# Kernel tuning notes

Measured on AMD Instinct MI355X. Metric: run time of the kernel, lower is better.

The kernel has to match this reference:

```python
import jax, jax.numpy as jnp
import numpy as np

N_PREV = 8191
DIMS = 4096


def setup_inputs() -> dict:
    key = jax.random.key(0)
    k1, k2, k3, k4, k5 = jax.random.split(key, 5)
    prev_inps = jax.random.normal(k1, (N_PREV, DIMS), dtype=jnp.float32)
    inp = jax.random.normal(k2, (DIMS,), dtype=jnp.float32)
    # learned parameters, init std=0.01 as in the torch module
    W_Q = jax.random.normal(k3, (DIMS, DIMS), dtype=jnp.float32) * 0.01
    W_K = jax.random.normal(k4, (DIMS, DIMS), dtype=jnp.float32) * 0.01
    W_V = jax.random.normal(k5, (DIMS, DIMS), dtype=jnp.float32) * 0.01
    return {"prev_inps": prev_inps, "inp": inp, "W_Q": W_Q, "W_K": W_K, "W_V": W_V}


def reference(prev_inps, inp, W_Q, W_K, W_V):
    # One masked self-attention decode step.
    inputs = jnp.concatenate([prev_inps, inp[None, :]], axis=0)  # (n+1, d)
    query = W_Q @ inp                                            # (d,)
    keys = jnp.einsum('md,nd->nm', W_K, inputs)                  # (n+1, d)
    values = jnp.einsum('md,nd->nm', W_V, inputs)                # (n+1, d)
    logits = keys @ query                                        # (n+1,)
    aweights = jax.nn.softmax(logits, axis=-1)                   # (n+1,)
    context = aweights @ values                                  # (d,)
    output = context + inp                                       # residual
    return (output, inputs)
```

## Files before the change

### kernel.cpp

```cpp
#include <hip/hip_runtime.h>
#include <math.h>

#define D      4096
#define NPREV  8191
#define NROWS  8192
#define FB     512
#define FR     (NROWS / FB)

typedef float f4 __attribute__((ext_vector_type(4)));

static __device__ __forceinline__ f4 nt_load4(const float* p) {
    return __builtin_nontemporal_load(reinterpret_cast<const f4*>(p));
}
static __device__ __forceinline__ void nt_store4(f4 v, float* p) {
    __builtin_nontemporal_store(v, reinterpret_cast<f4*>(p));
}
static __device__ __forceinline__ f4 ld4(const float* p) {
    return *reinterpret_cast<const f4*>(p);
}
static __device__ __forceinline__ void st4(f4 v, float* p) {
    *reinterpret_cast<f4*>(p) = v;
}

template<bool RESIDUAL>
__global__ void k_matvec_rows(const float* __restrict__ W, const float* __restrict__ v,
                              const float* __restrict__ resid, float* __restrict__ out) {
    int row  = blockIdx.x * 4 + (threadIdx.x >> 6);
    int lane = threadIdx.x & 63;
    const float* Wrow = W + (size_t)row * D;
    float acc = 0.f;
    #pragma unroll
    for (int i = 0; i < 16; ++i) {
        int c = lane + i * 64;
        f4 w = nt_load4(Wrow + 4 * c);
        f4 x = ld4(v + 4 * c);
        acc += w.x * x.x + w.y * x.y + w.z * x.z + w.w * x.w;
    }
    #pragma unroll
    for (int off = 32; off; off >>= 1) acc += __shfl_down(acc, off, 64);
    if (lane == 0) out[row] = RESIDUAL ? (acc + resid[row]) : acc;
}

__global__ void k_kq(const float* __restrict__ W, const float* __restrict__ q,
                     float* __restrict__ kq) {
    __shared__ float s_q[D];
    __shared__ f4 s_part[64][4];
    int t = threadIdx.x;
    int b = blockIdx.x;
    for (int i = t; i < D; i += 256) s_q[i] = q[i];
    __syncthreads();
    int c4 = b * 4 + (t & 3);
    int r0 = t >> 2;
    f4 acc = (f4)0.f;
    #pragma unroll 16
    for (int i = 0; i < 64; ++i) {
        int m = r0 + i * 64;
        acc += s_q[m] * nt_load4(W + (size_t)m * D + 4 * c4);
    }
    s_part[r0][t & 3] = acc;
    __syncthreads();
    if (t < 4) {
        f4 a = (f4)0.f;
        #pragma unroll
        for (int g = 0; g < 64; ++g) a += s_part[g][t];
        st4(a, kq + 4 * (b * 4 + t));
    }
}

__global__ __launch_bounds__(1024, 4) void k_flash(
        const float* __restrict__ prev, const float* __restrict__ inp,
        const float* __restrict__ kq, float* __restrict__ io,
        float* __restrict__ ms, float* __restrict__ ctxpart) {
    __shared__ float s_wred[16][FR];
    __shared__ float s_log[FR];
    const int n0 = blockIdx.x * FR;
    const int t = threadIdx.x;
    const int wid = t >> 6, lane = t & 63;
    const f4 kqv = ld4(kq + 4 * t);

    f4 x[FR];
    #pragma unroll
    for (int r = 0; r < FR; ++r) {
        int n = n0 + r;
        const float* src = (n < NPREV) ? (prev + (size_t)n * D) : inp;
        x[r] = ld4(src + 4 * t);
    }
    float p[FR];
    #pragma unroll
    for (int r = 0; r < FR; ++r) {
        int n = n0 + r;
        nt_store4(x[r], io + (size_t)n * D + 4 * t);
        p[r] = x[r].x * kqv.x + x[r].y * kqv.y + x[r].z * kqv.z + x[r].w * kqv.w;
    }
    #pragma unroll
    for (int r = 0; r < FR; ++r) {
        float v = p[r];
        #pragma unroll
        for (int off = 32; off; off >>= 1) v += __shfl_down(v, off, 64);
        if (lane == 0) s_wred[wid][r] = v;
    }
    __syncthreads();
    if (t < FR) {
        float s = 0.f;
        #pragma unroll
        for (int w = 0; w < 16; ++w) s += s_wred[w][t];
        s_log[t] = s;
    }
    __syncthreads();
    float m_b = -INFINITY;
    #pragma unroll
    for (int r = 0; r < FR; ++r) m_b = fmaxf(m_b, s_log[r]);
    float e[FR], s_b = 0.f;
    #pragma unroll
    for (int r = 0; r < FR; ++r) { e[r] = __expf(s_log[r] - m_b); s_b += e[r]; }
    f4 a = (f4)0.f;
    #pragma unroll
    for (int r = 0; r < FR; ++r) a += e[r] * x[r];
    st4(a, ctxpart + (size_t)blockIdx.x * D + 4 * t);
    if (t == 0) { ms[2 * blockIdx.x] = m_b; ms[2 * blockIdx.x + 1] = s_b; }
}

__global__ void k_combine(const float* __restrict__ ms, const float* __restrict__ ctxpart,
                          float* __restrict__ ctx) {
    __shared__ float s_w[FB];
    __shared__ float s_red[12];
    __shared__ f4 s_acc[8][32];
    int t = threadIdx.x;
    int lane = t & 63, wid = t >> 6;
    float m0 = ms[2 * t], m1 = ms[2 * (t + 256)];
    float mx = fmaxf(m0, m1);
    #pragma unroll
    for (int off = 32; off; off >>= 1) mx = fmaxf(mx, __shfl_down(mx, off, 64));
    if (lane == 0) s_red[wid] = mx;
    __syncthreads();
    float M = fmaxf(fmaxf(s_red[0], s_red[1]), fmaxf(s_red[2], s_red[3]));
    float w0 = __expf(m0 - M), w1 = __expf(m1 - M);
    s_w[t] = w0; s_w[t + 256] = w1;
    float sc = w0 * ms[2 * t + 1] + w1 * ms[2 * (t + 256) + 1];
    #pragma unroll
    for (int off = 32; off; off >>= 1) sc += __shfl_down(sc, off, 64);
    if (lane == 0) s_red[8 + wid] = sc;
    __syncthreads();
    float S = s_red[8] + s_red[9] + s_red[10] + s_red[11];
    int c  = t & 31;
    int g8 = t >> 5;
    int col4 = blockIdx.x * 32 + c;
    f4 a = (f4)0.f;
    #pragma unroll 8
    for (int i = 0; i < 64; ++i) {
        int p = g8 * 64 + i;
        a += s_w[p] * ld4(ctxpart + (size_t)p * D + 4 * col4);
    }
    s_acc[g8][c] = a;
    __syncthreads();
    if (t < 32) {
        f4 aa = (f4)0.f;
        #pragma unroll
        for (int g = 0; g < 8; ++g) aa += s_acc[g][t];
        st4(aa * (1.f / S), ctx + 4 * (blockIdx.x * 32 + t));
    }
}

extern "C" void kernel_launch(void* const* d_in, const int* in_sizes, int n_in,
                              void* d_out, int out_size, void* d_ws, size_t ws_size,
                              hipStream_t stream) {
    const float* prev = (const float*)d_in[0];
    const float* inp  = (const float*)d_in[1];
    const float* W_Q  = (const float*)d_in[2];
    const float* W_K  = (const float*)d_in[3];
    const float* W_V  = (const float*)d_in[4];
    float* out = (float*)d_out;
    float* io  = out + D;
    float* ws  = (float*)d_ws;

    float* q       = ws;
    float* kq      = q + D;
    float* ms      = kq + D;
    float* ctxpart = ms + 2 * FB;
    float* ctx     = ctxpart + (size_t)FB * D;

    k_matvec_rows<false><<<1024, 256, 0, stream>>>(W_Q, inp, nullptr, q);
    k_kq<<<256, 256, 0, stream>>>(W_K, q, kq);
    k_flash<<<FB, 1024, 0, stream>>>(prev, inp, kq, io, ms, ctxpart);
    k_combine<<<32, 256, 0, stream>>>(ms, ctxpart, ctx);
    k_matvec_rows<true><<<1024, 256, 0, stream>>>(W_V, ctx, inp, out);
}
```

Baseline: 116.0 us.

## Split flash pass into more, smaller LDS-staged blocks with workspace-size fallback

The flash-decode pass now uses 2048 blocks of 4 rows each instead of 512 blocks of 16. Rows are staged in shared memory rather than held in registers, and launch bounds allow 8 blocks per CU, aiming for more parallelism and memory-level concurrency on the large prev_inps read and write. The trade-off is 2048 partial context vectors (32 MB) to write and then read back in the combine kernel, which is generalised to a template and uses 64 blocks. If the workspace is too small, the old 16-row register path runs instead.

Result: faster. 112.5 us (-3.0%).

```diff
diff --git a/kernel.cpp b/kernel.cpp
--- a/kernel.cpp
+++ b/kernel.cpp
@@ -4,8 +4,6 @@
 #define D      4096
 #define NPREV  8191
 #define NROWS  8192
-#define FB     512
-#define FR     (NROWS / FB)
 
 typedef float f4 __attribute__((ext_vector_type(4)));
 
@@ -67,40 +65,98 @@
     }
 }
 
-__global__ __launch_bounds__(1024, 4) void k_flash(
+#define FBL  2048
+#define FRL  4
+__global__ __launch_bounds__(1024, 8) void k_flash_lds(
         const float* __restrict__ prev, const float* __restrict__ inp,
         const float* __restrict__ kq, float* __restrict__ io,
         float* __restrict__ ms, float* __restrict__ ctxpart) {
-    __shared__ float s_wred[16][FR];
-    __shared__ float s_log[FR];
-    const int n0 = blockIdx.x * FR;
+    __shared__ f4 s_x[FRL][1024];
+    __shared__ float s_wred[16][FRL];
+    __shared__ float s_log[FRL];
+    const int n0 = blockIdx.x * FRL;
     const int t = threadIdx.x;
     const int wid = t >> 6, lane = t & 63;
     const f4 kqv = ld4(kq + 4 * t);
 
-    f4 x[FR];
-    #pragma unroll
-    for (int r = 0; r < FR; ++r) {
+    f4 x[FRL];
+    #pragma unroll
+    for (int r = 0; r < FRL; ++r) {
         int n = n0 + r;
         const float* src = (n < NPREV) ? (prev + (size_t)n * D) : inp;
         x[r] = ld4(src + 4 * t);
     }
-    float p[FR];
-    #pragma unroll
-    for (int r = 0; r < FR; ++r) {
+    float p[FRL];
+    #pragma unroll
+    for (int r = 0; r < FRL; ++r) {
+        int n = n0 + r;
+        nt_store4(x[r], io + (size_t)n * D + 4 * t);
+        s_x[r][t] = x[r];
+        p[r] = x[r].x * kqv.x + x[r].y * kqv.y + x[r].z * kqv.z + x[r].w * kqv.w;
+    }
+    #pragma unroll
+    for (int r = 0; r < FRL; ++r) {
+        float v = p[r];
+        #pragma unroll
+        for (int off = 32; off; off >>= 1) v += __shfl_down(v, off, 64);
+        if (lane == 0) s_wred[wid][r] = v;
+    }
+    __syncthreads();
+    if (t < FRL) {
+        float s = 0.f;
+        #pragma unroll
+        for (int w = 0; w < 16; ++w) s += s_wred[w][t];
+        s_log[t] = s;
+    }
+    __syncthreads();
+    float m_b = -INFINITY;
+    #pragma unroll
+    for (int r = 0; r < FRL; ++r) m_b = fmaxf(m_b, s_log[r]);
+    float e[FRL], s_b = 0.f;
+    #pragma unroll
+    for (int r = 0; r < FRL; ++r) { e[r] = __expf(s_log[r] - m_b); s_b += e[r]; }
+    f4 a = (f4)0.f;
+    #pragma unroll
+    for (int r = 0; r < FRL; ++r) a += e[r] * s_x[r][t];
+    st4(a, ctxpart + (size_t)blockIdx.x * D + 4 * t);
+    if (t == 0) { ms[2 * blockIdx.x] = m_b; ms[2 * blockIdx.x + 1] = s_b; }
+}
+
+#define FBR  512
+#define FRR  16
+__global__ __launch_bounds__(1024, 4) void k_flash_reg(
+        const float* __restrict__ prev, const float* __restrict__ inp,
+        const float* __restrict__ kq, float* __restrict__ io,
+        float* __restrict__ ms, float* __restrict__ ctxpart) {
+    __shared__ float s_wred[16][FRR];
+    __shared__ float s_log[FRR];
+    const int n0 = blockIdx.x * FRR;
+    const int t = threadIdx.x;
+    const int wid = t >> 6, lane = t & 63;
+    const f4 kqv = ld4(kq + 4 * t);
+    f4 x[FRR];
+    #pragma unroll
+    for (int r = 0; r < FRR; ++r) {
+        int n = n0 + r;
+        const float* src = (n < NPREV) ? (prev + (size_t)n * D) : inp;
+        x[r] = ld4(src + 4 * t);
+    }
+    float p[FRR];
+    #pragma unroll
+    for (int r = 0; r < FRR; ++r) {
         int n = n0 + r;
         nt_store4(x[r], io + (size_t)n * D + 4 * t);
         p[r] = x[r].x * kqv.x + x[r].y * kqv.y + x[r].z * kqv.z + x[r].w * kqv.w;
     }
     #pragma unroll
-    for (int r = 0; r < FR; ++r) {
+    for (int r = 0; r < FRR; ++r) {
         float v = p[r];
         #pragma unroll
         for (int off = 32; off; off >>= 1) v += __shfl_down(v, off, 64);
         if (lane == 0) s_wred[wid][r] = v;
     }
     __syncthreads();
-    if (t < FR) {
+    if (t < FRR) {
         float s = 0.f;
         #pragma unroll
         for (int w = 0; w < 16; ++w) s += s_wred[w][t];
@@ -109,55 +165,63 @@
     __syncthreads();
     float m_b = -INFINITY;
     #pragma unroll
-    for (int r = 0; r < FR; ++r) m_b = fmaxf(m_b, s_log[r]);
-    float e[FR], s_b = 0.f;
-    #pragma unroll
-    for (int r = 0; r < FR; ++r) { e[r] = __expf(s_log[r] - m_b); s_b += e[r]; }
+    for (int r = 0; r < FRR; ++r) m_b = fmaxf(m_b, s_log[r]);
+    float e[FRR], s_b = 0.f;
+    #pragma unroll
+    for (int r = 0; r < FRR; ++r) { e[r] = __expf(s_log[r] - m_b); s_b += e[r]; }
     f4 a = (f4)0.f;
     #pragma unroll
-    for (int r = 0; r < FR; ++r) a += e[r] * x[r];
+    for (int r = 0; r < FRR; ++r) a += e[r] * x[r];
     st4(a, ctxpart + (size_t)blockIdx.x * D + 4 * t);
     if (t == 0) { ms[2 * blockIdx.x] = m_b; ms[2 * blockIdx.x + 1] = s_b; }
 }
 
+template<int FBT>
 __global__ void k_combine(const float* __restrict__ ms, const float* __restrict__ ctxpart,
                           float* __restrict__ ctx) {
-    __shared__ float s_w[FB];
-    __shared__ float s_red[12];
-    __shared__ f4 s_acc[8][32];
+    constexpr int PPT = FBT / 256;
+    constexpr int PPG = FBT / 16;
+    __shared__ float s_w[FBT];
+    __shared__ float s_red[8];
+    __shared__ f4 s_acc[16][16];
     int t = threadIdx.x;
     int lane = t & 63, wid = t >> 6;
-    float m0 = ms[2 * t], m1 = ms[2 * (t + 256)];
-    float mx = fmaxf(m0, m1);
+    float mloc[PPT];
+    float mx = -INFINITY;
+    #pragma unroll
+    for (int k = 0; k < PPT; ++k) { mloc[k] = ms[2 * (t + 256 * k)]; mx = fmaxf(mx, mloc[k]); }
     #pragma unroll
     for (int off = 32; off; off >>= 1) mx = fmaxf(mx, __shfl_down(mx, off, 64));
     if (lane == 0) s_red[wid] = mx;
     __syncthreads();
     float M = fmaxf(fmaxf(s_red[0], s_red[1]), fmaxf(s_red[2], s_red[3]));
-    float w0 = __expf(m0 - M), w1 = __expf(m1 - M);
-    s_w[t] = w0; s_w[t + 256] = w1;
-    float sc = w0 * ms[2 * t + 1] + w1 * ms[2 * (t + 256) + 1];
+    float sc = 0.f;
+    #pragma unroll
+    for (int k = 0; k < PPT; ++k) {
+        float w = __expf(mloc[k] - M);
+        s_w[t + 256 * k] = w;
+        sc += w * ms[2 * (t + 256 * k) + 1];
+    }
     #pragma unroll
     for (int off = 32; off; off >>= 1) sc += __shfl_down(sc, off, 64);
-    if (lane == 0) s_red[8 + wid] = sc;
-    __syncthreads();
-    float S = s_red[8] + s_red[9] + s_red[10] + s_red[11];
-    int c  = t & 31;
-    int g8 = t >> 5;
-    int col4 = blockIdx.x * 32 + c;
+    if (lane == 0) s_red[4 + wid] = sc;
+    __syncthreads();
+    float S = s_red[4] + s_red[5] + s_red[6] + s_red[7];
+    int c = t & 15, g = t >> 4;
+    int col4 = blockIdx.x * 16 + c;
     f4 a = (f4)0.f;
     #pragma unroll 8
-    for (int i = 0; i < 64; ++i) {
-        int p = g8 * 64 + i;
-        a += s_w[p] * ld4(ctxpart + (size_t)p * D + 4 * col4);
-    }
-    s_acc[g8][c] = a;
-    __syncthreads();
-    if (t < 32) {
+    for (int i = 0; i < PPG; ++i) {
+        int pp = g * PPG + i;
+        a += s_w[pp] * ld4(ctxpart + (size_t)pp * D + 4 * col4);
+    }
+    s_acc[g][c] = a;
+    __syncthreads();
+    if (t < 16) {
         f4 aa = (f4)0.f;
         #pragma unroll
-        for (int g = 0; g < 8; ++g) aa += s_acc[g][t];
-        st4(aa * (1.f / S), ctx + 4 * (blockIdx.x * 32 + t));
+        for (int gg = 0; gg < 16; ++gg) aa += s_acc[gg][t];
+        st4(aa * (1.f / S), ctx + 4 * (blockIdx.x * 16 + t));
     }
 }
 
@@ -173,15 +237,27 @@
     float* io  = out + D;
     float* ws  = (float*)d_ws;
 
-    float* q       = ws;
-    float* kq      = q + D;
-    float* ms      = kq + D;
-    float* ctxpart = ms + 2 * FB;
-    float* ctx     = ctxpart + (size_t)FB * D;
-
-    k_matvec_rows<false><<<1024, 256, 0, stream>>>(W_Q, inp, nullptr, q);
-    k_kq<<<256, 256, 0, stream>>>(W_K, q, kq);
-    k_flash<<<FB, 1024, 0, stream>>>(prev, inp, kq, io, ms, ctxpart);
-    k_combine<<<32, 256, 0, stream>>>(ms, ctxpart, ctx);
-    k_matvec_rows<true><<<1024, 256, 0, stream>>>(W_V, ctx, inp, out);
-}
+    size_t need_main = (size_t)(2 * D + 2 * FBL + (size_t)FBL * D + D) * sizeof(float);
+
+    float* q  = ws;
+    float* kq = q + D;
+    float* ms = kq + D;
+
+    if (ws_size >= need_main) {
+        float* ctxpart = ms + 2 * FBL;
+        float* ctx     = ctxpart + (size_t)FBL * D;
+        k_matvec_rows<false><<<1024, 256, 0, stream>>>(W_Q, inp, nullptr, q);
+        k_kq<<<256, 256, 0, stream>>>(W_K, q, kq);
+        k_flash_lds<<<FBL, 1024, 0, stream>>>(prev, inp, kq, io, ms, ctxpart);
+        k_combine<FBL><<<64, 256, 0, stream>>>(ms, ctxpart, ctx);
+        k_matvec_rows<true><<<1024, 256, 0, stream>>>(W_V, ctx, inp, out);
+    } else {
+        float* ctxpart = ms + 2 * FBR;
+        float* ctx     = ctxpart + (size_t)FBR * D;
+        k_matvec_rows<false><<<1024, 256, 0, stream>>>(W_Q, inp, nullptr, q);
+        k_kq<<<256, 256, 0, stream>>>(W_K, q, kq);
+        k_flash_reg<<<FBR, 1024, 0, stream>>>(prev, inp, kq, io, ms, ctxpart);
+        k_combine<FBR><<<64, 256, 0, stream>>>(ms, ctxpart, ctx);
+        k_matvec_rows<true><<<1024, 256, 0, stream>>>(W_V, ctx, inp, out);
+    }
+}
```

## Split flash kernel into separate copy and attention block roles

Applied to the files above, without the earlier changes.

Doubles the flash grid so half the blocks only copy rows into the concatenated output, while the other half compute logits and weighted context for the same row chunks. The attention blocks reload rows from memory (hopefully from cache) instead of holding 16 f4 values in registers, which relaxes register pressure and drops the nontemporal store. Combine is templated and uses 64 blocks with 16 columns each. The risk is that prev is read twice (copy blocks plus the attention pass and its reload), which could add DRAM traffic if the rows are not served from cache.

After: 126.8 us. +9.3%, slower.

```diff
diff --git a/kernel.cpp b/kernel.cpp
--- a/kernel.cpp
+++ b/kernel.cpp
@@ -5,15 +5,12 @@
 #define NPREV  8191
 #define NROWS  8192
 #define FB     512
-#define FR     (NROWS / FB)
+#define FR     16
 
 typedef float f4 __attribute__((ext_vector_type(4)));
 
 static __device__ __forceinline__ f4 nt_load4(const float* p) {
     return __builtin_nontemporal_load(reinterpret_cast<const f4*>(p));
-}
-static __device__ __forceinline__ void nt_store4(f4 v, float* p) {
-    __builtin_nontemporal_store(v, reinterpret_cast<f4*>(p));
 }
 static __device__ __forceinline__ f4 ld4(const float* p) {
     return *reinterpret_cast<const f4*>(p);
@@ -67,97 +64,119 @@
     }
 }
 
-__global__ __launch_bounds__(1024, 4) void k_flash(
+__global__ __launch_bounds__(1024) void k_flash_copy(
         const float* __restrict__ prev, const float* __restrict__ inp,
         const float* __restrict__ kq, float* __restrict__ io,
         float* __restrict__ ms, float* __restrict__ ctxpart) {
+    const int b    = blockIdx.x;
+    const int slot = b & 7;
+    const int grp  = b >> 3;
+    const int role = grp & 1;
+    const int wk   = (grp >> 1) * 8 + slot;
+    const int n0   = wk * FR;
+    const int t    = threadIdx.x;
+
+    if (role == 1) {
+        #pragma unroll 4
+        for (int r = 0; r < FR; ++r) {
+            int n = n0 + r;
+            const float* src = (n < NPREV) ? (prev + (size_t)n * D) : inp;
+            st4(ld4(src + 4 * t), io + (size_t)n * D + 4 * t);
+        }
+        return;
+    }
+
     __shared__ float s_wred[16][FR];
     __shared__ float s_log[FR];
-    const int n0 = blockIdx.x * FR;
-    const int t = threadIdx.x;
     const int wid = t >> 6, lane = t & 63;
     const f4 kqv = ld4(kq + 4 * t);
 
-    f4 x[FR];
+    float p[FR];
     #pragma unroll
     for (int r = 0; r < FR; ++r) {
         int n = n0 + r;
         const float* src = (n < NPREV) ? (prev + (size_t)n * D) : inp;
-        x[r] = ld4(src + 4 * t);
-    }
-    float p[FR];
+        f4 x = ld4(src + 4 * t);
+        p[r] = x.x * kqv.x + x.y * kqv.y + x.z * kqv.z + x.w * kqv.w;
+    }
+    #pragma unroll
+    for (int r = 0; r < FR; ++r) {
+        float v = p[r];
+        #pragma unroll
+        for (int off = 32; off; off >>= 1) v += __shfl_down(v, off, 64);
+        if (lane == 0) s_wred[wid][r] = v;
+    }
+    __syncthreads();
+    if (t < FR) {
+        float s = 0.f;
+        #pragma unroll
+        for (int w = 0; w < 16; ++w) s += s_wred[w][t];
+        s_log[t] = s;
+    }
+    __syncthreads();
+    float m_b = -INFINITY;
+    #pragma unroll
+    for (int r = 0; r < FR; ++r) m_b = fmaxf(m_b, s_log[r]);
+    float e[FR], s_b = 0.f;
+    #pragma unroll
+    for (int r = 0; r < FR; ++r) { e[r] = __expf(s_log[r] - m_b); s_b += e[r]; }
+    f4 a = (f4)0.f;
     #pragma unroll
     for (int r = 0; r < FR; ++r) {
         int n = n0 + r;
-        nt_store4(x[r], io + (size_t)n * D + 4 * t);
-        p[r] = x[r].x * kqv.x + x[r].y * kqv.y + x[r].z * kqv.z + x[r].w * kqv.w;
-    }
-    #pragma unroll
-    for (int r = 0; r < FR; ++r) {
-        float v = p[r];
-        #pragma unroll
-        for (int off = 32; off; off >>= 1) v += __shfl_down(v, off, 64);
-        if (lane == 0) s_wred[wid][r] = v;
-    }
-    __syncthreads();
-    if (t < FR) {
-        float s = 0.f;
-        #pragma unroll
-        for (int w = 0; w < 16; ++w) s += s_wred[w][t];
-        s_log[t] = s;
-    }
-    __syncthreads();
-    float m_b = -INFINITY;
-    #pragma unroll
-    for (int r = 0; r < FR; ++r) m_b = fmaxf(m_b, s_log[r]);
-    float e[FR], s_b = 0.f;
-    #pragma unroll
-    for (int r = 0; r < FR; ++r) { e[r] = __expf(s_log[r] - m_b); s_b += e[r]; }
-    f4 a = (f4)0.f;
-    #pragma unroll
-    for (int r = 0; r < FR; ++r) a += e[r] * x[r];
-    st4(a, ctxpart + (size_t)blockIdx.x * D + 4 * t);
-    if (t == 0) { ms[2 * blockIdx.x] = m_b; ms[2 * blockIdx.x + 1] = s_b; }
-}
-
+        const float* src = (n < NPREV) ? (prev + (size_t)n * D) : inp;
+        a += e[r] * ld4(src + 4 * t);
+    }
+    st4(a, ctxpart + (size_t)wk * D + 4 * t);
+    if (t == 0) { ms[2 * wk] = m_b; ms[2 * wk + 1] = s_b; }
+}
+
+template<int FBT>
 __global__ void k_combine(const float* __restrict__ ms, const float* __restrict__ ctxpart,
                           float* __restrict__ ctx) {
-    __shared__ float s_w[FB];
-    __shared__ float s_red[12];
-    __shared__ f4 s_acc[8][32];
+    constexpr int PPT = FBT / 256;
+    constexpr int PPG = FBT / 16;
+    __shared__ float s_w[FBT];
+    __shared__ float s_red[8];
+    __shared__ f4 s_acc[16][16];
     int t = threadIdx.x;
     int lane = t & 63, wid = t >> 6;
-    float m0 = ms[2 * t], m1 = ms[2 * (t + 256)];
-    float mx = fmaxf(m0, m1);
+    float mloc[PPT];
+    float mx = -INFINITY;
+    #pragma unroll
+    for (int k = 0; k < PPT; ++k) { mloc[k] = ms[2 * (t + 256 * k)]; mx = fmaxf(mx, mloc[k]); }
     #pragma unroll
     for (int off = 32; off; off >>= 1) mx = fmaxf(mx, __shfl_down(mx, off, 64));
     if (lane == 0) s_red[wid] = mx;
     __syncthreads();
     float M = fmaxf(fmaxf(s_red[0], s_red[1]), fmaxf(s_red[2], s_red[3]));
-    float w0 = __expf(m0 - M), w1 = __expf(m1 - M);
-    s_w[t] = w0; s_w[t + 256] = w1;
-    float sc = w0 * ms[2 * t + 1] + w1 * ms[2 * (t + 256) + 1];
+    float sc = 0.f;
+    #pragma unroll
+    for (int k = 0; k < PPT; ++k) {
+        float w = __expf(mloc[k] - M);
+        s_w[t + 256 * k] = w;
+        sc += w * ms[2 * (t + 256 * k) + 1];
+    }
     #pragma unroll
     for (int off = 32; off; off >>= 1) sc += __shfl_down(sc, off, 64);
-    if (lane == 0) s_red[8 + wid] = sc;
-    __syncthreads();
-    float S = s_red[8] + s_red[9] + s_red[10] + s_red[11];
-    int c  = t & 31;
-    int g8 = t >> 5;
-    int col4 = blockIdx.x * 32 + c;
+    if (lane == 0) s_red[4 + wid] = sc;
+    __syncthreads();
+    float S = s_red[4] + s_red[5] + s_red[6] + s_red[7];
+    int c = t & 15, g = t >> 4;
+    int col4 = blockIdx.x * 16 + c;
     f4 a = (f4)0.f;
     #pragma unroll 8
-    for (int i = 0; i < 64; ++i) {
-        int p = g8 * 64 + i;
-        a += s_w[p] * ld4(ctxpart + (size_t)p * D + 4 * col4);
-    }
-    s_acc[g8][c] = a;
-    __syncthreads();
-    if (t < 32) {
+    for (int i = 0; i < PPG; ++i) {
+        int pp = g * PPG + i;
+        a += s_w[pp] * ld4(ctxpart + (size_t)pp * D + 4 * col4);
+    }
+    s_acc[g][c] = a;
+    __syncthreads();
+    if (t < 16) {
         f4 aa = (f4)0.f;
         #pragma unroll
-        for (int g = 0; g < 8; ++g) aa += s_acc[g][t];
-        st4(aa * (1.f / S), ctx + 4 * (blockIdx.x * 32 + t));
+        for (int gg = 0; gg < 16; ++gg) aa += s_acc[gg][t];
+        st4(aa * (1.f / S), ctx + 4 * (blockIdx.x * 16 + t));
     }
 }
 
@@ -181,7 +200,7 @@
 
     k_matvec_rows<false><<<1024, 256, 0, stream>>>(W_Q, inp, nullptr, q);
     k_kq<<<256, 256, 0, stream>>>(W_K, q, kq);
-    k_flash<<<FB, 1024, 0, stream>>>(prev, inp, kq, io, ms, ctxpart);
-    k_combine<<<32, 256, 0, stream>>>(ms, ctxpart, ctx);
+    k_flash_copy<<<1024, 1024, 0, stream>>>(prev, inp, kq, io, ms, ctxpart);
+    k_combine<FB><<<64, 256, 0, stream>>>(ms, ctxpart, ctx);
     k_matvec_rows<true><<<1024, 256, 0, stream>>>(W_V, ctx, inp, out);
 }
```
